# Optimization experiments

Hardware: AMD Instinct MI355X
Metric: run time of the kernel (lower is better)

The kernel has to match this reference:

```python
import jax, jax.numpy as jnp
import numpy as np

B, T, FEA, H, OUT, L = 40, 20, 200, 1024, 1095, 12


def setup_inputs() -> dict:
    key = jax.random.key(0)
    ks = jax.random.split(key, 8)

    def init(k, shape, fan_in):
        return jax.random.normal(k, shape, jnp.float32) * (1.0 / np.sqrt(fan_in))

    return {
        "x": jax.random.normal(ks[0], (B, T, FEA), jnp.float32),
        "hidden": jnp.zeros((L, B, H), jnp.float32),  # initial SRU cell state c0 per layer
        "W1": init(ks[1], (FEA, H), FEA),
        "b1": jnp.zeros((H,), jnp.float32),
        "sru_W": init(ks[2], (L, H, 3 * H), H),   # per layer: [x_tilde | f-gate | r-gate]
        "sru_b": jnp.zeros((L, 2 * H), jnp.float32),  # per layer: [b_f | b_r]
        "W3": init(ks[3], (H, H), H),
        "b3": jnp.zeros((H,), jnp.float32),
        "W4": init(ks[4], (H, OUT), H),
        "b4": jnp.zeros((OUT,), jnp.float32),
    }


def _sru_layer(x, c0, W, b):
    # x: [t, b, h]; SRU (Lei et al. 2017) with use_tanh=True and highway on x
    U = jnp.einsum('tbh,hk->tbk', x, W)          # [t, b, 3h]
    x_tilde, uf, ur = jnp.split(U, 3, axis=-1)
    bf, br = jnp.split(b, 2)
    f = jax.nn.sigmoid(uf + bf)                  # forget gate
    r = jax.nn.sigmoid(ur + br)                  # reset/highway gate

    def step(c, ins):
        ft, xt = ins
        c = ft * c + (1.0 - ft) * xt
        return c, c

    c_last, cs = jax.lax.scan(step, c0, (f, x_tilde))
    h = r * jnp.tanh(cs) + (1.0 - r) * x
    return h, c_last


def reference(x, hidden, W1, b1, sru_W, sru_b, W3, b3, W4, b4):
    b, t, _ = x.shape
    # Dense_layer1 (dropout is identity at inference)
    h = jnp.dot(x.reshape(b * t, -1), W1) + b1
    h = h.reshape(b, t, H).transpose(1, 0, 2)    # [t, b, H] (time-major for SRU)
    c_finals = []
    for l in range(sru_W.shape[0]):
        h, c_l = _sru_layer(h, hidden[l], sru_W[l], sru_b[l])
        c_finals.append(c_l)
    hidden_after = jnp.stack(c_finals)           # [L, b, H]
    h = h.transpose(1, 0, 2).reshape(b * t, H)
    h = jax.nn.relu(jnp.dot(h, W3) + b3)
    out = jnp.dot(h, W4) + b4                    # [b*t, OUT]
    return out, hidden_after
```

## Files before the change

kernel.cpp:

```cpp
#include <hip/hip_runtime.h>
#include <hip/hip_bf16.h>
#include <math.h>

typedef __bf16 bf16_t;
typedef __bf16 bf16x8 __attribute__((ext_vector_type(8)));
typedef float f32x4 __attribute__((ext_vector_type(4)));
typedef unsigned short u16;

#define NB   40
#define NT   20
#define FEA  200
#define HD   1024
#define NOUT 1095
#define NL   12
#define M_ROWS 800
#define LDSB 34816
#define UPITCH 196

__global__ __launch_bounds__(256)
void transpose_convert(const float* __restrict__ src, bf16_t* __restrict__ dst,
                       int srcK, int srcN, int Kp, int Np)
{
    __shared__ u16 tile[64 * 66];
    const int t = threadIdx.x;
    src += (size_t)blockIdx.z * srcK * srcN;
    dst += (size_t)blockIdx.z * Np * Kp;
    const int n0 = blockIdx.x << 6, k0 = blockIdx.y << 6;
    {
        const int nl = t & 63, kb = (t >> 6) << 4;
        const int gn = n0 + nl;
        #pragma unroll
        for (int j = 0; j < 16; j++) {
            const int gk = k0 + kb + j;
            float v = (gk < srcK && gn < srcN) ? src[(size_t)gk * srcN + gn] : 0.f;
            bf16_t b = (bf16_t)v;
            tile[nl * 66 + kb + j] = *(const u16*)&b;
        }
    }
    __syncthreads();
    {
        const int nl = t >> 2, kg = (t & 3) << 4;
        const unsigned* tp = (const unsigned*)tile;
        const int dw = nl * 33 + (kg >> 1);
        uint4 v0, v1;
        v0.x = tp[dw+0]; v0.y = tp[dw+1]; v0.z = tp[dw+2]; v0.w = tp[dw+3];
        v1.x = tp[dw+4]; v1.y = tp[dw+5]; v1.z = tp[dw+6]; v1.w = tp[dw+7];
        bf16_t* dp = dst + (size_t)(n0 + nl) * Kp + k0 + kg;
        *(uint4*)dp = v0;
        *(uint4*)(dp + 8) = v1;
    }
}

__global__ __launch_bounds__(256)
void convert_pad_x(const float* __restrict__ src, bf16_t* __restrict__ dst)
{
    const int m = blockIdx.x, k = threadIdx.x;
    dst[m * 256 + k] = (bf16_t)((k < FEA) ? src[(size_t)m * FEA + k] : 0.f);
}

template<bool OUT_F32, bool RELU>
__global__ __launch_bounds__(256)
void gemm_tiled(const bf16_t* __restrict__ A, const bf16_t* __restrict__ Bt,
                const float* __restrict__ bias, void* __restrict__ C,
                int M, int Nstore, int Ks)
{
    __shared__ char lds[2][24576];
    const int tid = threadIdx.x;
    const int w = tid >> 6, lane = tid & 63, quad = lane >> 4, l16 = lane & 15;
    const int n0 = blockIdx.x << 6;
    const int m0 = blockIdx.y << 7;
    const int wr = w >> 1, wc = w & 1;

    const int lrow  = lane >> 3;
    const int gslot = ((lane & 7) ^ lrow) << 3;
    const bf16_t* aSrc[4];
    const bf16_t* bSrc[2];
    #pragma unroll
    for (int i = 0; i < 4; i++) {
        int r = m0 + (w * 4 + i) * 8 + lrow;
        if (r > M - 1) r = M - 1;
        aSrc[i] = A + (size_t)r * Ks + gslot;
    }
    #pragma unroll
    for (int i = 0; i < 2; i++)
        bSrc[i] = Bt + (size_t)(n0 + (w * 2 + i) * 8 + lrow) * Ks + gslot;

    f32x4 acc[4][2];
    #pragma unroll
    for (int m = 0; m < 4; m++)
        #pragma unroll
        for (int n = 0; n < 2; n++) acc[m][n] = (f32x4){0.f, 0.f, 0.f, 0.f};

    const int nkt = Ks >> 6;

    #define STAGE(p, kt) do {                                                  \
        const int _k0 = (kt) << 6;                                             \
        char* _b = &lds[p][0];                                                 \
        _Pragma("unroll")                                                      \
        for (int _i = 0; _i < 4; _i++)                                         \
            __builtin_amdgcn_global_load_lds(                                  \
                (const __attribute__((address_space(1))) void*)(aSrc[_i] + _k0),\
                (__attribute__((address_space(3))) void*)(_b + (w * 4 + _i) * 1024), \
                16, 0, 0);                                                     \
        _Pragma("unroll")                                                      \
        for (int _i = 0; _i < 2; _i++)                                         \
            __builtin_amdgcn_global_load_lds(                                  \
                (const __attribute__((address_space(1))) void*)(bSrc[_i] + _k0),\
                (__attribute__((address_space(3))) void*)(_b + 16384 + (w * 2 + _i) * 1024), \
                16, 0, 0);                                                     \
    } while (0)

    STAGE(0, 0);
    __syncthreads();

    for (int kt = 0; kt < nkt; kt++) {
        const int p = kt & 1;
        if (kt + 1 < nkt) STAGE(p ^ 1, kt + 1);
        const char* ab = &lds[p][0];
        #pragma unroll
        for (int kk = 0; kk < 2; kk++) {
            const int ts = (kk << 2) + quad;
            bf16x8 a[4], b[2];
            #pragma unroll
            for (int m = 0; m < 4; m++) {
                const int r = wr * 64 + m * 16 + l16;
                a[m] = *(const bf16x8*)(ab + r * 128 + ((ts ^ (r & 7)) << 4));
            }
            #pragma unroll
            for (int n = 0; n < 2; n++) {
                const int r = wc * 32 + n * 16 + l16;
                b[n] = *(const bf16x8*)(ab + 16384 + r * 128 + ((ts ^ (r & 7)) << 4));
            }
            #pragma unroll
            for (int m = 0; m < 4; m++)
                #pragma unroll
                for (int n = 0; n < 2; n++)
                    acc[m][n] = __builtin_amdgcn_mfma_f32_16x16x32_bf16(a[m], b[n], acc[m][n], 0, 0, 0);
        }
        __syncthreads();
    }
    #undef STAGE

    #pragma unroll
    for (int n = 0; n < 2; n++) {
        const int col = n0 + wc * 32 + n * 16 + l16;
        if (col >= Nstore) continue;
        const float bv = bias ? bias[col] : 0.f;
        #pragma unroll
        for (int m = 0; m < 4; m++) {
            #pragma unroll
            for (int i = 0; i < 4; i++) {
                const int mg = m0 + wr * 64 + m * 16 + quad * 4 + i;
                if (mg < M) {
                    float v = acc[m][n][i] + bv;
                    if (RELU) v = v > 0.f ? v : 0.f;
                    if (OUT_F32) ((float*)C)[(size_t)mg * Nstore + col] = v;
                    else         ((bf16_t*)C)[(size_t)mg * Nstore + col] = (bf16_t)v;
                }
            }
        }
    }
}

__global__ __launch_bounds__(256)
void sru_layer_fused(const bf16_t* __restrict__ hin, bf16_t* __restrict__ hout,
                     const bf16_t* __restrict__ Wt, const float* __restrict__ c0,
                     const float* __restrict__ bvec, float* __restrict__ cout)
{
    extern __shared__ char lds_raw[];
    const int tid = threadIdx.x;
    const int w = tid >> 6, lane = tid & 63, quad = lane >> 4, l16 = lane & 15;
    const int n0 = blockIdx.x << 6;
    const int m0 = blockIdx.y * 80;

    const int lrow  = lane >> 3;
    const int gslot = ((lane & 7) ^ lrow) << 3;

    const bf16_t* aSrc[3];
    #pragma unroll
    for (int i = 0; i < 3; i++) {
        int r = (w * 3 + i) * 8 + lrow;
        if (r > 79) r = 79;
        aSrc[i] = hin + (size_t)(m0 + r) * HD + gslot;
    }
    const bf16_t* bSrc[6];
    #pragma unroll
    for (int i = 0; i < 6; i++) {
        const int r = (w * 6 + i) * 8 + lrow;
        bSrc[i] = Wt + (size_t)((r >> 6) * HD + n0 + (r & 63)) * HD + gslot;
    }

    f32x4 acc[5][3];
    #pragma unroll
    for (int m = 0; m < 5; m++)
        #pragma unroll
        for (int n = 0; n < 3; n++) acc[m][n] = (f32x4){0.f, 0.f, 0.f, 0.f};

    #define STAGE(p, kt) do {                                                  \
        const int _k0 = (kt) << 6;                                             \
        char* _b = lds_raw + (p) * LDSB;                                       \
        _Pragma("unroll")                                                      \
        for (int _i = 0; _i < 3; _i++)                                         \
            if (w * 3 + _i < 10)                                               \
                __builtin_amdgcn_global_load_lds(                              \
                    (const __attribute__((address_space(1))) void*)(aSrc[_i] + _k0), \
                    (__attribute__((address_space(3))) void*)(_b + (w * 3 + _i) * 1024), \
                    16, 0, 0);                                                 \
        _Pragma("unroll")                                                      \
        for (int _i = 0; _i < 6; _i++)                                         \
            __builtin_amdgcn_global_load_lds(                                  \
                (const __attribute__((address_space(1))) void*)(bSrc[_i] + _k0), \
                (__attribute__((address_space(3))) void*)(_b + 10240 + (w * 6 + _i) * 1024), \
                16, 0, 0);                                                     \
    } while (0)

    STAGE(0, 0);
    __syncthreads();

    for (int kt = 0; kt < 16; kt++) {
        const int p = kt & 1;
        if (kt < 15) STAGE(p ^ 1, kt + 1);
        const char* ab = lds_raw + p * LDSB;
        const char* bb = ab + 10240;
        #pragma unroll
        for (int kk = 0; kk < 2; kk++) {
            const int ts = (kk << 2) + quad;
            bf16x8 a[5], b[3];
            #pragma unroll
            for (int m = 0; m < 5; m++) {
                const int r = m * 16 + l16;
                a[m] = *(const bf16x8*)(ab + r * 128 + ((ts ^ (r & 7)) << 4));
            }
            #pragma unroll
            for (int n = 0; n < 3; n++) {
                const int r = (w * 3 + n) * 16 + l16;
                b[n] = *(const bf16x8*)(bb + r * 128 + ((ts ^ (r & 7)) << 4));
            }
            #pragma unroll
            for (int m = 0; m < 5; m++)
                #pragma unroll
                for (int n = 0; n < 3; n++)
                    acc[m][n] = __builtin_amdgcn_mfma_f32_16x16x32_bf16(a[m], b[n], acc[m][n], 0, 0, 0);
        }
        __syncthreads();
    }
    #undef STAGE

    float* Ul = (float*)lds_raw;
    #pragma unroll
    for (int m = 0; m < 5; m++)
        #pragma unroll
        for (int n = 0; n < 3; n++) {
            const int col = (w * 3 + n) * 16 + l16;
            #pragma unroll
            for (int i = 0; i < 4; i++)
                Ul[(m * 16 + quad * 4 + i) * UPITCH + col] = acc[m][n][i];
        }
    __syncthreads();

    const int bl = tid >> 6, nn = tid & 63, bg = blockIdx.y * 4 + bl;
    float c = c0[(size_t)bg * HD + n0 + nn];
    const float bfb = bvec[n0 + nn], brb = bvec[HD + n0 + nn];
    for (int t = 0; t < NT; t++) {
        const float* u = &Ul[(bl * NT + t) * UPITCH];
        const float xt = u[nn];
        const float uf = u[64 + nn];
        const float ur = u[128 + nn];
        const float f = 1.f / (1.f + __expf(-(uf + bfb)));
        const float r = 1.f / (1.f + __expf(-(ur + brb)));
        c = f * c + (1.f - f) * xt;
        const size_t gi = (size_t)(bg * NT + t) * HD + n0 + nn;
        const float hp = (float)hin[gi];
        hout[gi] = (bf16_t)(r * tanhf(c) + (1.f - r) * hp);
    }
    cout[(size_t)bg * HD + n0 + nn] = c;
}

extern "C" void kernel_launch(void* const* d_in, const int* in_sizes, int n_in,
                              void* d_out, int out_size, void* d_ws, size_t ws_size,
                              hipStream_t stream)
{
    const float* x      = (const float*)d_in[0];
    const float* hidden = (const float*)d_in[1];
    const float* W1     = (const float*)d_in[2];
    const float* b1     = (const float*)d_in[3];
    const float* sruW   = (const float*)d_in[4];
    const float* srub   = (const float*)d_in[5];
    const float* W3     = (const float*)d_in[6];
    const float* b3     = (const float*)d_in[7];
    const float* W4     = (const float*)d_in[8];
    const float* b4     = (const float*)d_in[9];

    float* out     = (float*)d_out;
    float* hid_out = out + (size_t)M_ROWS * NOUT;

    bf16_t* h0 = (bf16_t*)d_out;

    hipFuncSetAttribute((const void*)sru_layer_fused,
                        hipFuncAttributeMaxDynamicSharedMemorySize, 2 * LDSB);

    char* ws = (char*)d_ws;
    const size_t SZ_WT  = (size_t)NL * 3 * HD * HD * 2;
    const size_t SZ_W1  = (size_t)HD * 256 * 2;
    const size_t SZ_W3  = (size_t)HD * HD * 2;
    const size_t SZ_W4  = (size_t)1152 * HD * 2;
    const size_t SZ_XB  = (size_t)M_ROWS * 256 * 2;
    const size_t SZ_H   = (size_t)M_ROWS * HD * 2;
    const size_t SLOT   = (size_t)3 * HD * HD * 2;
    const size_t FAST_NEED = SZ_WT + SZ_W1 + SZ_W3 + SZ_W4 + SZ_XB + 2 * SZ_H;
    const bool fast = ws_size >= FAST_NEED;

    const dim3 blk(256);
    const int GY = (M_ROWS + 127) >> 7;

    if (fast) {
        bf16_t* wt  = (bf16_t*)ws;
        bf16_t* w1t = (bf16_t*)(ws + SZ_WT);
        bf16_t* w3t = (bf16_t*)(ws + SZ_WT + SZ_W1);
        bf16_t* w4t = (bf16_t*)(ws + SZ_WT + SZ_W1 + SZ_W3);
        bf16_t* xb  = (bf16_t*)(ws + SZ_WT + SZ_W1 + SZ_W3 + SZ_W4);
        bf16_t* h1  = (bf16_t*)(ws + SZ_WT + SZ_W1 + SZ_W3 + SZ_W4 + SZ_XB);
        bf16_t* g   = (bf16_t*)(ws + SZ_WT + SZ_W1 + SZ_W3 + SZ_W4 + SZ_XB + SZ_H);

        convert_pad_x<<<M_ROWS, blk, 0, stream>>>(x, xb);
        transpose_convert<<<dim3(16, 4, 1),  blk, 0, stream>>>(W1,   w1t, FEA, HD,    256, HD);
        transpose_convert<<<dim3(48, 16, NL), blk, 0, stream>>>(sruW, wt,  HD,  3*HD, HD,  3*HD);
        transpose_convert<<<dim3(16, 16, 1), blk, 0, stream>>>(W3,   w3t, HD,  HD,   HD,  HD);
        transpose_convert<<<dim3(18, 16, 1), blk, 0, stream>>>(W4,   w4t, HD,  NOUT, HD,  1152);

        gemm_tiled<false, false><<<dim3(16, GY), blk, 0, stream>>>(xb, w1t, b1, h0, M_ROWS, HD, 256);

        for (int l = 0; l < NL; l++) {
            const bf16_t* hi = (l & 1) ? h1 : h0;
            bf16_t*       ho = (l & 1) ? h0 : h1;
            sru_layer_fused<<<dim3(16, 10), blk, 2 * LDSB, stream>>>(
                hi, ho, wt + (size_t)l * 3 * HD * HD,
                hidden + (size_t)l * NB * HD, srub + (size_t)l * 2 * HD,
                hid_out + (size_t)l * NB * HD);
        }
        gemm_tiled<false, true><<<dim3(16, GY), blk, 0, stream>>>(h0, w3t, b3, g, M_ROWS, HD, HD);
        gemm_tiled<true, false><<<dim3(18, GY), blk, 0, stream>>>(g, w4t, b4, out, M_ROWS, NOUT, HD);
    } else {
        bf16_t* slot = (bf16_t*)ws;
        bf16_t* xb   = (bf16_t*)(ws + SLOT);
        bf16_t* h1   = (bf16_t*)(ws + SLOT + SZ_XB);
        bf16_t* g    = (bf16_t*)(ws + SLOT + SZ_XB + SZ_H);

        convert_pad_x<<<M_ROWS, blk, 0, stream>>>(x, xb);
        transpose_convert<<<dim3(16, 4, 1), blk, 0, stream>>>(W1, slot, FEA, HD, 256, HD);
        gemm_tiled<false, false><<<dim3(16, GY), blk, 0, stream>>>(xb, slot, b1, h0, M_ROWS, HD, 256);

        for (int l = 0; l < NL; l++) {
            transpose_convert<<<dim3(48, 16, 1), blk, 0, stream>>>(
                sruW + (size_t)l * HD * 3 * HD, slot, HD, 3*HD, HD, 3*HD);
            const bf16_t* hi = (l & 1) ? h1 : h0;
            bf16_t*       ho = (l & 1) ? h0 : h1;
            sru_layer_fused<<<dim3(16, 10), blk, 2 * LDSB, stream>>>(
                hi, ho, slot,
                hidden + (size_t)l * NB * HD, srub + (size_t)l * 2 * HD,
                hid_out + (size_t)l * NB * HD);
        }
        transpose_convert<<<dim3(16, 16, 1), blk, 0, stream>>>(W3, slot, HD, HD, HD, HD);
        gemm_tiled<false, true><<<dim3(16, GY), blk, 0, stream>>>(h0, slot, b3, g, M_ROWS, HD, HD);
        transpose_convert<<<dim3(18, 16, 1), blk, 0, stream>>>(W4, slot, HD, NOUT, HD, 1152);
        gemm_tiled<true, false><<<dim3(18, GY), blk, 0, stream>>>(g, slot, b4, out, M_ROWS, NOUT, HD);
    }
}
```

Baseline: 551.9 us.

## Deepen GEMM and SRU LDS pipelines to four buffers with vmcnt-based waits

Both the generic GEMM and the fused SRU layer kernel move from double-buffered LDS staging to a 4-slot ring with prefetch distance 2. The per-iteration __syncthreads is replaced by explicit s_waitcnt vmcnt counts plus a single s_barrier. The aim is to keep more global-to-LDS loads in flight and hide memory latency. It raises LDS usage (about 144KB for SRU, 96KB for GEMM), which lowers occupancy. Removing the trailing barrier and the A-row guard (A loads now always issue, rows clamped) relies on the ring depth to avoid overwriting slots still being read.

New measurement: 544.5 us. Within noise of the previous version (-1.3%).

```diff
diff --git a/kernel.cpp b/kernel.cpp
--- a/kernel.cpp
+++ b/kernel.cpp
@@ -14,8 +14,10 @@
 #define NOUT 1095
 #define NL   12
 #define M_ROWS 800
-#define LDSB 34816
 #define UPITCH 196
+
+#define FBUF 36864
+#define GBUF 24576
 
 __global__ __launch_bounds__(256)
 void transpose_convert(const float* __restrict__ src, bf16_t* __restrict__ dst,
@@ -64,7 +66,7 @@
                 const float* __restrict__ bias, void* __restrict__ C,
                 int M, int Nstore, int Ks)
 {
-    __shared__ char lds[2][24576];
+    extern __shared__ char lds[];
     const int tid = threadIdx.x;
     const int w = tid >> 6, lane = tid & 63, quad = lane >> 4, l16 = lane & 15;
     const int n0 = blockIdx.x << 6;
@@ -93,9 +95,9 @@
 
     const int nkt = Ks >> 6;
 
-    #define STAGE(p, kt) do {                                                  \
+    #define STAGE(kt) do {                                                     \
         const int _k0 = (kt) << 6;                                             \
-        char* _b = &lds[p][0];                                                 \
+        char* _b = lds + ((kt) & 3) * GBUF;                                    \
         _Pragma("unroll")                                                      \
         for (int _i = 0; _i < 4; _i++)                                         \
             __builtin_amdgcn_global_load_lds(                                  \
@@ -110,13 +112,18 @@
                 16, 0, 0);                                                     \
     } while (0)
 
-    STAGE(0, 0);
-    __syncthreads();
+    STAGE(0);
+    if (nkt > 1) STAGE(1);
 
     for (int kt = 0; kt < nkt; kt++) {
-        const int p = kt & 1;
-        if (kt + 1 < nkt) STAGE(p ^ 1, kt + 1);
-        const char* ab = &lds[p][0];
+        if (kt + 2 < nkt) STAGE(kt + 2);
+        const int rem = nkt - 1 - kt;
+        if (rem >= 2)      asm volatile("s_waitcnt vmcnt(12)" ::: "memory");
+        else if (rem == 1) asm volatile("s_waitcnt vmcnt(6)"  ::: "memory");
+        else               asm volatile("s_waitcnt vmcnt(0)"  ::: "memory");
+        __builtin_amdgcn_s_barrier();
+
+        const char* ab = lds + (kt & 3) * GBUF;
         #pragma unroll
         for (int kk = 0; kk < 2; kk++) {
             const int ts = (kk << 2) + quad;
@@ -137,7 +144,6 @@
                 for (int n = 0; n < 2; n++)
                     acc[m][n] = __builtin_amdgcn_mfma_f32_16x16x32_bf16(a[m], b[n], acc[m][n], 0, 0, 0);
         }
-        __syncthreads();
     }
     #undef STAGE
 
@@ -196,32 +202,36 @@
         #pragma unroll
         for (int n = 0; n < 3; n++) acc[m][n] = (f32x4){0.f, 0.f, 0.f, 0.f};
 
-    #define STAGE(p, kt) do {                                                  \
+    #define STAGEF(kt) do {                                                    \
         const int _k0 = (kt) << 6;                                             \
-        char* _b = lds_raw + (p) * LDSB;                                       \
+        char* _b = lds_raw + ((kt) & 3) * FBUF;                                \
         _Pragma("unroll")                                                      \
         for (int _i = 0; _i < 3; _i++)                                         \
-            if (w * 3 + _i < 10)                                               \
-                __builtin_amdgcn_global_load_lds(                              \
-                    (const __attribute__((address_space(1))) void*)(aSrc[_i] + _k0), \
-                    (__attribute__((address_space(3))) void*)(_b + (w * 3 + _i) * 1024), \
-                    16, 0, 0);                                                 \
+            __builtin_amdgcn_global_load_lds(                                  \
+                (const __attribute__((address_space(1))) void*)(aSrc[_i] + _k0), \
+                (__attribute__((address_space(3))) void*)(_b + (w * 3 + _i) * 1024), \
+                16, 0, 0);                                                     \
         _Pragma("unroll")                                                      \
         for (int _i = 0; _i < 6; _i++)                                         \
             __builtin_amdgcn_global_load_lds(                                  \
                 (const __attribute__((address_space(1))) void*)(bSrc[_i] + _k0), \
-                (__attribute__((address_space(3))) void*)(_b + 10240 + (w * 6 + _i) * 1024), \
+                (__attribute__((address_space(3))) void*)(_b + 12288 + (w * 6 + _i) * 1024), \
                 16, 0, 0);                                                     \
     } while (0)
 
-    STAGE(0, 0);
-    __syncthreads();
+    STAGEF(0);
+    STAGEF(1);
 
     for (int kt = 0; kt < 16; kt++) {
-        const int p = kt & 1;
-        if (kt < 15) STAGE(p ^ 1, kt + 1);
-        const char* ab = lds_raw + p * LDSB;
-        const char* bb = ab + 10240;
+        if (kt + 2 < 16) STAGEF(kt + 2);
+        const int rem = 15 - kt;
+        if (rem >= 2)      asm volatile("s_waitcnt vmcnt(18)" ::: "memory");
+        else if (rem == 1) asm volatile("s_waitcnt vmcnt(9)"  ::: "memory");
+        else               asm volatile("s_waitcnt vmcnt(0)"  ::: "memory");
+        __builtin_amdgcn_s_barrier();
+
+        const char* ab = lds_raw + (kt & 3) * FBUF;
+        const char* bb = ab + 12288;
         #pragma unroll
         for (int kk = 0; kk < 2; kk++) {
             const int ts = (kk << 2) + quad;
@@ -242,9 +252,8 @@
                 for (int n = 0; n < 3; n++)
                     acc[m][n] = __builtin_amdgcn_mfma_f32_16x16x32_bf16(a[m], b[n], acc[m][n], 0, 0, 0);
         }
-        __syncthreads();
-    }
-    #undef STAGE
+    }
+    #undef STAGEF
 
     float* Ul = (float*)lds_raw;
     #pragma unroll
@@ -297,7 +306,13 @@
     bf16_t* h0 = (bf16_t*)d_out;
 
     hipFuncSetAttribute((const void*)sru_layer_fused,
-                        hipFuncAttributeMaxDynamicSharedMemorySize, 2 * LDSB);
+                        hipFuncAttributeMaxDynamicSharedMemorySize, 4 * FBUF);
+    hipFuncSetAttribute((const void*)gemm_tiled<false, false>,
+                        hipFuncAttributeMaxDynamicSharedMemorySize, 4 * GBUF);
+    hipFuncSetAttribute((const void*)gemm_tiled<false, true>,
+                        hipFuncAttributeMaxDynamicSharedMemorySize, 4 * GBUF);
+    hipFuncSetAttribute((const void*)gemm_tiled<true, false>,
+                        hipFuncAttributeMaxDynamicSharedMemorySize, 4 * GBUF);
 
     char* ws = (char*)d_ws;
     const size_t SZ_WT  = (size_t)NL * 3 * HD * HD * 2;
@@ -328,18 +343,18 @@
         transpose_convert<<<dim3(16, 16, 1), blk, 0, stream>>>(W3,   w3t, HD,  HD,   HD,  HD);
         transpose_convert<<<dim3(18, 16, 1), blk, 0, stream>>>(W4,   w4t, HD,  NOUT, HD,  1152);
 
-        gemm_tiled<false, false><<<dim3(16, GY), blk, 0, stream>>>(xb, w1t, b1, h0, M_ROWS, HD, 256);
+        gemm_tiled<false, false><<<dim3(16, GY), blk, 4 * GBUF, stream>>>(xb, w1t, b1, h0, M_ROWS, HD, 256);
 
         for (int l = 0; l < NL; l++) {
             const bf16_t* hi = (l & 1) ? h1 : h0;
             bf16_t*       ho = (l & 1) ? h0 : h1;
-            sru_layer_fused<<<dim3(16, 10), blk, 2 * LDSB, stream>>>(
+            sru_layer_fused<<<dim3(16, 10), blk, 4 * FBUF, stream>>>(
                 hi, ho, wt + (size_t)l * 3 * HD * HD,
                 hidden + (size_t)l * NB * HD, srub + (size_t)l * 2 * HD,
                 hid_out + (size_t)l * NB * HD);
         }
-        gemm_tiled<false, true><<<dim3(16, GY), blk, 0, stream>>>(h0, w3t, b3, g, M_ROWS, HD, HD);
-        gemm_tiled<true, false><<<dim3(18, GY), blk, 0, stream>>>(g, w4t, b4, out, M_ROWS, NOUT, HD);
+        gemm_tiled<false, true><<<dim3(16, GY), blk, 4 * GBUF, stream>>>(h0, w3t, b3, g, M_ROWS, HD, HD);
+        gemm_tiled<true, false><<<dim3(18, GY), blk, 4 * GBUF, stream>>>(g, w4t, b4, out, M_ROWS, NOUT, HD);
     } else {
         bf16_t* slot = (bf16_t*)ws;
         bf16_t* xb   = (bf16_t*)(ws + SLOT);
@@ -348,21 +363,21 @@
 
         convert_pad_x<<<M_ROWS, blk, 0, stream>>>(x, xb);
         transpose_convert<<<dim3(16, 4, 1), blk, 0, stream>>>(W1, slot, FEA, HD, 256, HD);
-        gemm_tiled<false, false><<<dim3(16, GY), blk, 0, stream>>>(xb, slot, b1, h0, M_ROWS, HD, 256);
+        gemm_tiled<false, false><<<dim3(16, GY), blk, 4 * GBUF, stream>>>(xb, slot, b1, h0, M_ROWS, HD, 256);
 
         for (int l = 0; l < NL; l++) {
             transpose_convert<<<dim3(48, 16, 1), blk, 0, stream>>>(
                 sruW + (size_t)l * HD * 3 * HD, slot, HD, 3*HD, HD, 3*HD);
             const bf16_t* hi = (l & 1) ? h1 : h0;
             bf16_t*       ho = (l & 1) ? h0 : h1;
-            sru_layer_fused<<<dim3(16, 10), blk, 2 * LDSB, stream>>>(
+            sru_layer_fused<<<dim3(16, 10), blk, 4 * FBUF, stream>>>(
                 hi, ho, slot,
                 hidden + (size_t)l * NB * HD, srub + (size_t)l * 2 * HD,
                 hid_out + (size_t)l * NB * HD);
         }
         transpose_convert<<<dim3(16, 16, 1), blk, 0, stream>>>(W3, slot, HD, HD, HD, HD);
-        gemm_tiled<false, true><<<dim3(16, GY), blk, 0, stream>>>(h0, slot, b3, g, M_ROWS, HD, HD);
+        gemm_tiled<false, true><<<dim3(16, GY), blk, 4 * GBUF, stream>>>(h0, slot, b3, g, M_ROWS, HD, HD);
         transpose_convert<<<dim3(18, 16, 1), blk, 0, stream>>>(W4, slot, HD, NOUT, HD, 1152);
-        gemm_tiled<true, false><<<dim3(18, GY), blk, 0, stream>>>(g, slot, b4, out, M_ROWS, NOUT, HD);
-    }
-}
+        gemm_tiled<true, false><<<dim3(18, GY), blk, 4 * GBUF, stream>>>(g, slot, b4, out, M_ROWS, NOUT, HD);
+    }
+}
```
